# Kernel optimization log

Hardware: AMD Instinct MI355X
Metric: run time of the kernel (lower is better)

The kernel has to match this reference:

```python
import jax, jax.numpy as jnp
import numpy as np

T, D, R = 8192, 2048, 2048

def setup_inputs() -> dict:
    key = jax.random.key(0)
    ks = jax.random.split(key, 5)
    x = jax.random.normal(ks[0], (T, D), jnp.float32)
    h0 = jnp.zeros((R,), jnp.float32)  # initialize_carry()
    W_a = jax.random.normal(ks[1], (D, R), jnp.float32) / np.float32(np.sqrt(D))
    W_b = jax.random.normal(ks[2], (D, R), jnp.float32) / np.float32(np.sqrt(D))
    W_out = jax.random.normal(ks[3], (R, D), jnp.float32) / np.float32(np.sqrt(R))
    W_skip = jax.random.normal(ks[4], (D, D), jnp.float32) / np.float32(np.sqrt(D))
    return {"x": x, "h0": h0, "W_a": W_a, "W_b": W_b, "W_out": W_out, "W_skip": W_skip}


def _combine(e1, e2):
    # semigroup op for diagonal linear recurrence: h' = a2*h + b2
    a1, b1 = e1
    a2, b2 = e2
    return (a1 * a2, a2 * b1 + b2)


def reference(x, h0, W_a, W_b, W_out, W_skip):
    # forward_map (vmapped over time via broadcasting): x_t -> (a_t, b_t)
    a = jax.nn.sigmoid(x @ W_a)        # [T, R] input-dependent decay
    b = (x @ W_b) * (1.0 - a)          # [T, R] gated input injection
    # fold initial carry in as identity-decay element (1, h0), then scan
    ones_row = jnp.ones((1, R), x.dtype)
    a_all = jnp.concatenate([ones_row, a], axis=0)          # [T+1, R]
    b_all = jnp.concatenate([h0[None, :], b], axis=0)       # [T+1, R]
    _, h_all = jax.lax.associative_scan(_combine, (a_all, b_all), axis=0)
    next_h = h_all[1:]                 # [T, R] recurrent states
    # backward_map (vmapped over time): h_t, x_t -> y_t
    y = jnp.tanh(next_h) @ W_out + x @ W_skip   # [T, D]
    return next_h, y
```

## Files before the change

### kernel.cpp

```cpp
#include <hip/hip_runtime.h>
#include <hip/hip_fp16.h>


#define T_DIM 8192
#define D_DIM 2048
#define R_DIM 2048
#define NCH   128
#define LCH   64

typedef _Float16 f16;
typedef _Float16 f16x2 __attribute__((ext_vector_type(2)));
typedef _Float16 f16x4 __attribute__((ext_vector_type(4)));
typedef _Float16 f16x8 __attribute__((ext_vector_type(8)));
typedef float    f32x4 __attribute__((ext_vector_type(4)));

#define AS1 __attribute__((address_space(1)))
#define AS3 __attribute__((address_space(3)))
#define GLOAD_LDS16(g, l) \
  __builtin_amdgcn_global_load_lds((const AS1 void*)(g), (AS3 void*)(l), 16, 0, 0)

__device__ __forceinline__ int swz(int p) { return p ^ (((p >> 7) & 7) << 4); }


__global__ __launch_bounds__(256) void cvt_f32_f16_kernel(
    const float* __restrict__ in, f16* __restrict__ out, int n4) {
  int i = blockIdx.x * 256 + threadIdx.x;
  if (i >= n4) return;
  float4 v = ((const float4*)in)[i];
  f16x4 o; o.x = (f16)v.x; o.y = (f16)v.y; o.z = (f16)v.z; o.w = (f16)v.w;
  ((f16x4*)out)[i] = o;
}

__global__ __launch_bounds__(256) void transpose_cvt_kernel(
    const float* __restrict__ in, f16* __restrict__ out) {
  __shared__ float tile[32][33];
  int bx = blockIdx.x * 32, by = blockIdx.y * 32;
  int tx = threadIdx.x, ty = threadIdx.y;
  #pragma unroll
  for (int i = 0; i < 32; i += 8)
    tile[ty + i][tx] = in[(size_t)(by + ty + i) * 2048 + bx + tx];
  __syncthreads();
  #pragma unroll
  for (int i = 0; i < 32; i += 8)
    out[(size_t)(bx + ty + i) * 2048 + by + tx] = (f16)tile[tx][ty + i];
}

template <int MODE>
__global__ __launch_bounds__(512, 2) void gemm_kernel(
    const f16* __restrict__ A1, const f16* __restrict__ B1, int NT1,
    const f16* __restrict__ A2, const f16* __restrict__ B2, int NT2,
    const f16* __restrict__ aAux, void* __restrict__ outp) {
  __shared__ __align__(16) char lds[4 * 32768];
  const int tid = threadIdx.x;
  const int l = tid & 63, w = tid >> 6;
  const int wrow = w >> 2, wcol = w & 3;
  const int l15 = l & 15, kq = (l >> 4) * 16;

  const int id = blockIdx.x;
  const int sw = (id & 7) * 32 + (id >> 3);
  const int m0 = (sw >> 3) * 256, n0 = (sw & 7) * 256;
  const int NTtot = NT1 + NT2;

  int gOff[2];
  #pragma unroll
  for (int q = 0; q < 2; q++) {
    int p = (q * 512 + tid) * 16 & 16383;
    int lg = swz(p);
    gOff[q] = (lg >> 6) * 4096 + (lg & 63);
  }
  int oA[8], oB[4];
  #pragma unroll
  for (int m = 0; m < 8; m++)
    oA[m] = swz((wrow * 128 + m * 16 + l15) * 64 + kq);
  #pragma unroll
  for (int n = 0; n < 4; n++)
    oB[n] = swz((wcol * 64 + n * 16 + l15) * 64 + kq);

  f32x4 acc[8][4];
  #pragma unroll
  for (int m = 0; m < 8; m++)
    #pragma unroll
    for (int n = 0; n < 4; n++)
      acc[m][n] = (f32x4){0.f, 0.f, 0.f, 0.f};

  auto stage = [&](int tf) {
    const f16* At; const f16* Bt; int kt;
    if (tf < NT1) { At = A1; Bt = B1; kt = tf; }
    else          { At = A2; Bt = B2; kt = tf - NT1; }
    const char* gA = (const char*)(At + (size_t)m0 * 2048 + kt * 32);
    const char* gB = (const char*)(Bt + (size_t)n0 * 2048 + kt * 32);
    char* ldsA = lds + (tf & 3) * 32768;
    char* ldsB = ldsA + 16384;
    #pragma unroll
    for (int q = 0; q < 2; q++) {
      GLOAD_LDS16(gA + gOff[q], ldsA + (q * 512 + w * 64) * 16);
      GLOAD_LDS16(gB + gOff[q], ldsB + (q * 512 + w * 64) * 16);
    }
  };

  stage(0); stage(1); stage(2);

  for (int t = 0; t < NTtot; ++t) {
    const int rem = NTtot - 1 - t;
    if (rem >= 2)      asm volatile("s_waitcnt vmcnt(8)" ::: "memory");
    else if (rem == 1) asm volatile("s_waitcnt vmcnt(4)" ::: "memory");
    else               asm volatile("s_waitcnt vmcnt(0)" ::: "memory");
    asm volatile("s_barrier" ::: "memory");
    if (t + 3 < NTtot) stage(t + 3);

    const char* bA = lds + (t & 3) * 32768;
    const char* bB = bA + 16384;
    f16x8 af[8], bf[4];
    #pragma unroll
    for (int m = 0; m < 8; m++) af[m] = *(const f16x8*)(bA + oA[m]);
    #pragma unroll
    for (int n = 0; n < 4; n++) bf[n] = *(const f16x8*)(bB + oB[n]);
    __builtin_amdgcn_s_setprio(1);
    #pragma unroll
    for (int m = 0; m < 8; m++)
      #pragma unroll
      for (int n = 0; n < 4; n++)
        acc[m][n] = __builtin_amdgcn_mfma_f32_16x16x32_f16(af[m], bf[n], acc[m][n], 0, 0, 0);
    __builtin_amdgcn_s_setprio(0);
  }

  const int r0 = m0 + wrow * 128 + (l >> 4) * 4;
  const int c0 = n0 + wcol * 64 + l15;
  #pragma unroll
  for (int m = 0; m < 8; m++)
    #pragma unroll
    for (int n = 0; n < 4; n++)
      #pragma unroll
      for (int j = 0; j < 4; j++) {
        size_t idx = (size_t)(r0 + m * 16 + j) * 2048 + (c0 + n * 16);
        float v = acc[m][n][j];
        if (MODE == 0) {
          ((float*)outp)[idx] = v;
        } else if (MODE == 1) {
          ((f16*)outp)[idx] = (f16)(1.0f / (1.0f + __expf(-v)));
        } else {
          ((f16*)outp)[idx] = (f16)(v * (1.0f - (float)aAux[idx]));
        }
      }
}


__global__ __launch_bounds__(256) void scan_pass_a(
    const f16* __restrict__ a, const f16* __restrict__ b,
    float* __restrict__ Ac, float* __restrict__ Bc) {
  int tid = blockIdx.x * 256 + threadIdx.x;
  int c  = tid >> 10;
  int r2 = (tid & 1023) << 1;
  const f16* pa = a + (size_t)c * LCH * R_DIM + r2;
  const f16* pb = b + (size_t)c * LCH * R_DIM + r2;
  float A0 = 1.f, B0 = 0.f, A1 = 1.f, B1 = 0.f;
  #pragma unroll 8
  for (int i = 0; i < LCH; i++) {
    f16x2 av = *(const f16x2*)(pa + (size_t)i * R_DIM);
    f16x2 bv = *(const f16x2*)(pb + (size_t)i * R_DIM);
    float a0 = (float)av.x, a1 = (float)av.y;
    B0 = fmaf(a0, B0, (float)bv.x); A0 *= a0;
    B1 = fmaf(a1, B1, (float)bv.y); A1 *= a1;
  }
  size_t o = (size_t)c * R_DIM + r2;
  *(float2*)&Ac[o] = make_float2(A0, A1);
  *(float2*)&Bc[o] = make_float2(B0, B1);
}

__global__ __launch_bounds__(256) void scan_carry(
    const float* __restrict__ Ac, const float* __restrict__ Bc,
    const float* __restrict__ h0, float* __restrict__ carry) {
  int r = blockIdx.x * 256 + threadIdx.x;
  float h = h0[r];
  #pragma unroll 8
  for (int c = 0; c < NCH; c++) {
    size_t o = (size_t)c * R_DIM + r;
    carry[o] = h;
    h = fmaf(Ac[o], h, Bc[o]);
  }
}

__global__ __launch_bounds__(256) void scan_pass_c(
    const f16* __restrict__ a, const f16* __restrict__ b,
    const float* __restrict__ carry,
    float* __restrict__ hout, f16* __restrict__ th) {
  int tid = blockIdx.x * 256 + threadIdx.x;
  int c  = tid >> 10;
  int r2 = (tid & 1023) << 1;
  size_t base = (size_t)c * LCH * R_DIM + r2;
  const f16* pa = a + base;
  const f16* pb = b + base;
  float2 hv = *(const float2*)&carry[(size_t)c * R_DIM + r2];
  float hA = hv.x, hB = hv.y;
  #pragma unroll 4
  for (int i = 0; i < LCH; i++) {
    f16x2 av = *(const f16x2*)(pa + (size_t)i * R_DIM);
    f16x2 bv = *(const f16x2*)(pb + (size_t)i * R_DIM);
    hA = fmaf((float)av.x, hA, (float)bv.x);
    hB = fmaf((float)av.y, hB, (float)bv.y);
    size_t o = base + (size_t)i * R_DIM;
    *(float2*)&hout[o] = make_float2(hA, hB);
    f16x2 tv; tv.x = (f16)tanhf(hA); tv.y = (f16)tanhf(hB);
    *(f16x2*)(th + o) = tv;
  }
}


extern "C" void kernel_launch(void* const* d_in, const int* in_sizes, int n_in,
                              void* d_out, int out_size, void* d_ws, size_t ws_size,
                              hipStream_t stream) {
  const float* x      = (const float*)d_in[0];
  const float* h0     = (const float*)d_in[1];
  const float* W_a    = (const float*)d_in[2];
  const float* W_b    = (const float*)d_in[3];
  const float* W_out  = (const float*)d_in[4];
  const float* W_skip = (const float*)d_in[5];
  float* out_h = (float*)d_out;
  float* out_y = out_h + (size_t)T_DIM * R_DIM;

  char* ws = (char*)d_ws;
  size_t off = 0;
  auto alloc = [&](size_t bytes) -> void* {
    void* p = ws + off;
    off += (bytes + 255) & ~(size_t)255;
    return p;
  };
  f16*  x16   = (f16*)alloc((size_t)T_DIM * D_DIM * 2);
  f16*  WaT   = (f16*)alloc((size_t)D_DIM * R_DIM * 2);
  f16*  WbT   = (f16*)alloc((size_t)D_DIM * R_DIM * 2);
  f16*  WoutT = (f16*)alloc((size_t)R_DIM * D_DIM * 2);
  f16*  WskT  = (f16*)alloc((size_t)D_DIM * D_DIM * 2);
  f16*  a16   = (f16*)alloc((size_t)T_DIM * R_DIM * 2);
  f16*  b16   = (f16*)alloc((size_t)T_DIM * R_DIM * 2);
  f16*  th16  = (f16*)alloc((size_t)T_DIM * R_DIM * 2);
  float* Ac   = (float*)alloc((size_t)NCH * R_DIM * 4);
  float* Bc   = (float*)alloc((size_t)NCH * R_DIM * 4);
  float* carry= (float*)alloc((size_t)NCH * R_DIM * 4);

  {
    int n4 = T_DIM * D_DIM / 4;
    cvt_f32_f16_kernel<<<(n4 + 255) / 256, 256, 0, stream>>>(x, x16, n4);
  }
  dim3 tg(64, 64), tb(32, 8);
  transpose_cvt_kernel<<<tg, tb, 0, stream>>>(W_a,    WaT);
  transpose_cvt_kernel<<<tg, tb, 0, stream>>>(W_b,    WbT);
  transpose_cvt_kernel<<<tg, tb, 0, stream>>>(W_out,  WoutT);
  transpose_cvt_kernel<<<tg, tb, 0, stream>>>(W_skip, WskT);

  const int NT = D_DIM / 32;
  gemm_kernel<1><<<256, 512, 0, stream>>>(x16, WaT, NT, nullptr, nullptr, 0, nullptr, a16);
  gemm_kernel<2><<<256, 512, 0, stream>>>(x16, WbT, NT, nullptr, nullptr, 0, a16,    b16);

  scan_pass_a<<<NCH * (R_DIM / 2) / 256, 256, 0, stream>>>(a16, b16, Ac, Bc);
  scan_carry <<<R_DIM / 256, 256, 0, stream>>>(Ac, Bc, h0, carry);
  scan_pass_c<<<NCH * (R_DIM / 2) / 256, 256, 0, stream>>>(a16, b16, carry, out_h, th16);

  gemm_kernel<0><<<256, 512, 0, stream>>>(th16, WoutT, NT, x16, WskT, NT, nullptr, out_y);
}
```

Baseline: 563.1 us.

## Retile GEMM to 32x32 MFMA with 256x128 tiles and move gating into scan

The GEMM now uses 256x128 block tiles with 32x32x16 MFMAs, triple-buffered LDS and an occupancy target of four blocks. Its epilogue stores raw pre-activations in f16, so the sigmoid and gating are recomputed inside both scan passes and the GEMM no longer rereads the gate tensor. The four weight transposes are merged into one launch, and tanh/sigmoid use fast rcp/exp forms. This cuts launch count and epilogue traffic in exchange for smaller tiles, recomputed transcendentals in the scans, and a possible loss of precision from storing pre-activations in f16.

```diff
diff --git a/kernel.cpp b/kernel.cpp
--- a/kernel.cpp
+++ b/kernel.cpp
@@ -12,7 +12,7 @@
 typedef _Float16 f16x2 __attribute__((ext_vector_type(2)));
 typedef _Float16 f16x4 __attribute__((ext_vector_type(4)));
 typedef _Float16 f16x8 __attribute__((ext_vector_type(8)));
-typedef float    f32x4 __attribute__((ext_vector_type(4)));
+typedef float    f32x16 __attribute__((ext_vector_type(16)));
 
 #define AS1 __attribute__((address_space(1)))
 #define AS3 __attribute__((address_space(3)))
@@ -20,6 +20,13 @@
   __builtin_amdgcn_global_load_lds((const AS1 void*)(g), (AS3 void*)(l), 16, 0, 0)
 
 __device__ __forceinline__ int swz(int p) { return p ^ (((p >> 7) & 7) << 4); }
+
+__device__ __forceinline__ float sigmoid_f(float z) {
+  return __builtin_amdgcn_rcpf(1.0f + __expf(-z));
+}
+__device__ __forceinline__ float tanh_f(float x) {
+  return 1.0f - 2.0f * __builtin_amdgcn_rcpf(1.0f + __expf(2.0f * x));
+}
 
 
 __global__ __launch_bounds__(256) void cvt_f32_f16_kernel(
@@ -32,7 +39,16 @@
 }
 
 __global__ __launch_bounds__(256) void transpose_cvt_kernel(
-    const float* __restrict__ in, f16* __restrict__ out) {
+    const float* __restrict__ s0, f16* __restrict__ d0,
+    const float* __restrict__ s1, f16* __restrict__ d1,
+    const float* __restrict__ s2, f16* __restrict__ d2,
+    const float* __restrict__ s3, f16* __restrict__ d3) {
+  const float* in; f16* out;
+  int z = blockIdx.z;
+  if (z == 0)      { in = s0; out = d0; }
+  else if (z == 1) { in = s1; out = d1; }
+  else if (z == 2) { in = s2; out = d2; }
+  else             { in = s3; out = d3; }
   __shared__ float tile[32][33];
   int bx = blockIdx.x * 32, by = blockIdx.y * 32;
   int tx = threadIdx.x, ty = threadIdx.y;
@@ -46,121 +62,127 @@
 }
 
 template <int MODE>
-__global__ __launch_bounds__(512, 2) void gemm_kernel(
+__global__ __launch_bounds__(512, 4) void gemm_kernel(
     const f16* __restrict__ A1, const f16* __restrict__ B1, int NT1,
     const f16* __restrict__ A2, const f16* __restrict__ B2, int NT2,
-    const f16* __restrict__ aAux, void* __restrict__ outp) {
-  __shared__ __align__(16) char lds[4 * 32768];
+    void* __restrict__ outp) {
+  __shared__ __align__(16) char lds[3 * 24576];
   const int tid = threadIdx.x;
   const int l = tid & 63, w = tid >> 6;
-  const int wrow = w >> 2, wcol = w & 3;
-  const int l15 = l & 15, kq = (l >> 4) * 16;
+  const int wrow = w >> 1, wcol = w & 1;
+  const int l31 = l & 31, hi = l >> 5;
 
   const int id = blockIdx.x;
-  const int sw = (id & 7) * 32 + (id >> 3);
-  const int m0 = (sw >> 3) * 256, n0 = (sw & 7) * 256;
+  const int sw = (id & 7) * 64 + (id >> 3);
+  const int m0 = (sw >> 4) * 256, n0 = (sw & 15) * 128;
   const int NTtot = NT1 + NT2;
 
-  int gOff[2];
-  #pragma unroll
-  for (int q = 0; q < 2; q++) {
-    int p = (q * 512 + tid) * 16 & 16383;
-    int lg = swz(p);
-    gOff[q] = (lg >> 6) * 4096 + (lg & 63);
-  }
-  int oA[8], oB[4];
-  #pragma unroll
-  for (int m = 0; m < 8; m++)
-    oA[m] = swz((wrow * 128 + m * 16 + l15) * 64 + kq);
-  #pragma unroll
-  for (int n = 0; n < 4; n++)
-    oB[n] = swz((wcol * 64 + n * 16 + l15) * 64 + kq);
-
-  f32x4 acc[8][4];
-  #pragma unroll
-  for (int m = 0; m < 8; m++)
-    #pragma unroll
-    for (int n = 0; n < 4; n++)
-      acc[m][n] = (f32x4){0.f, 0.f, 0.f, 0.f};
-
-  auto stage = [&](int tf) {
+  int gA0, gA1, gB0;
+  {
+    int p0 = tid * 16;
+    int p1 = (512 + tid) * 16;
+    int pb = tid * 16;
+    int lg;
+    lg = swz(p0); gA0 = (lg >> 6) * 4096 + (lg & 63);
+    lg = swz(p1); gA1 = (lg >> 6) * 4096 + (lg & 63);
+    lg = swz(pb); gB0 = (lg >> 6) * 4096 + (lg & 63);
+  }
+  int oA[2][2], oB[2][2];
+  #pragma unroll
+  for (int m = 0; m < 2; m++)
+    #pragma unroll
+    for (int kk = 0; kk < 2; kk++)
+      oA[m][kk] = swz((wrow * 64 + m * 32 + l31) * 64 + kk * 32 + hi * 16);
+  #pragma unroll
+  for (int n = 0; n < 2; n++)
+    #pragma unroll
+    for (int kk = 0; kk < 2; kk++)
+      oB[n][kk] = swz((wcol * 64 + n * 32 + l31) * 64 + kk * 32 + hi * 16);
+
+  f32x16 acc[2][2];
+  #pragma unroll
+  for (int m = 0; m < 2; m++)
+    #pragma unroll
+    for (int n = 0; n < 2; n++)
+      #pragma unroll
+      for (int r = 0; r < 16; r++)
+        acc[m][n][r] = 0.f;
+
+  auto stage = [&](int tf, int slot) {
     const f16* At; const f16* Bt; int kt;
     if (tf < NT1) { At = A1; Bt = B1; kt = tf; }
     else          { At = A2; Bt = B2; kt = tf - NT1; }
-    const char* gA = (const char*)(At + (size_t)m0 * 2048 + kt * 32);
-    const char* gB = (const char*)(Bt + (size_t)n0 * 2048 + kt * 32);
-    char* ldsA = lds + (tf & 3) * 32768;
-    char* ldsB = ldsA + 16384;
-    #pragma unroll
-    for (int q = 0; q < 2; q++) {
-      GLOAD_LDS16(gA + gOff[q], ldsA + (q * 512 + w * 64) * 16);
-      GLOAD_LDS16(gB + gOff[q], ldsB + (q * 512 + w * 64) * 16);
-    }
+    const char* gA = (const char*)At + (size_t)m0 * 4096 + kt * 64;
+    const char* gB = (const char*)Bt + (size_t)n0 * 4096 + kt * 64;
+    char* dA = lds + slot * 24576;
+    char* dB = dA + 16384;
+    GLOAD_LDS16(gA + gA0, dA + (w * 64) * 16);
+    GLOAD_LDS16(gA + gA1, dA + (512 + w * 64) * 16);
+    GLOAD_LDS16(gB + gB0, dB + (w * 64) * 16);
   };
 
-  stage(0); stage(1); stage(2);
-
+  stage(0, 0); stage(1, 1);
+  int cs = 0;
   for (int t = 0; t < NTtot; ++t) {
-    const int rem = NTtot - 1 - t;
-    if (rem >= 2)      asm volatile("s_waitcnt vmcnt(8)" ::: "memory");
-    else if (rem == 1) asm volatile("s_waitcnt vmcnt(4)" ::: "memory");
+    if (t < NTtot - 1) asm volatile("s_waitcnt vmcnt(3)" ::: "memory");
     else               asm volatile("s_waitcnt vmcnt(0)" ::: "memory");
     asm volatile("s_barrier" ::: "memory");
-    if (t + 3 < NTtot) stage(t + 3);
-
-    const char* bA = lds + (t & 3) * 32768;
+    if (t + 2 < NTtot) {
+      int ss = cs + 2; if (ss >= 3) ss -= 3;
+      stage(t + 2, ss);
+    }
+    const char* bA = lds + cs * 24576;
     const char* bB = bA + 16384;
-    f16x8 af[8], bf[4];
-    #pragma unroll
-    for (int m = 0; m < 8; m++) af[m] = *(const f16x8*)(bA + oA[m]);
-    #pragma unroll
-    for (int n = 0; n < 4; n++) bf[n] = *(const f16x8*)(bB + oB[n]);
     __builtin_amdgcn_s_setprio(1);
     #pragma unroll
-    for (int m = 0; m < 8; m++)
+    for (int kk = 0; kk < 2; kk++) {
+      f16x8 a0 = *(const f16x8*)(bA + oA[0][kk]);
+      f16x8 a1 = *(const f16x8*)(bA + oA[1][kk]);
+      f16x8 b0 = *(const f16x8*)(bB + oB[0][kk]);
+      f16x8 b1 = *(const f16x8*)(bB + oB[1][kk]);
+      acc[0][0] = __builtin_amdgcn_mfma_f32_32x32x16_f16(a0, b0, acc[0][0], 0, 0, 0);
+      acc[0][1] = __builtin_amdgcn_mfma_f32_32x32x16_f16(a0, b1, acc[0][1], 0, 0, 0);
+      acc[1][0] = __builtin_amdgcn_mfma_f32_32x32x16_f16(a1, b0, acc[1][0], 0, 0, 0);
+      acc[1][1] = __builtin_amdgcn_mfma_f32_32x32x16_f16(a1, b1, acc[1][1], 0, 0, 0);
+    }
+    __builtin_amdgcn_s_setprio(0);
+    cs = (cs == 2) ? 0 : cs + 1;
+  }
+
+  const int r0 = m0 + wrow * 64 + 4 * hi;
+  const int c0 = n0 + wcol * 64 + l31;
+  #pragma unroll
+  for (int m = 0; m < 2; m++)
+    #pragma unroll
+    for (int n = 0; n < 2; n++)
       #pragma unroll
-      for (int n = 0; n < 4; n++)
-        acc[m][n] = __builtin_amdgcn_mfma_f32_16x16x32_f16(af[m], bf[n], acc[m][n], 0, 0, 0);
-    __builtin_amdgcn_s_setprio(0);
-  }
-
-  const int r0 = m0 + wrow * 128 + (l >> 4) * 4;
-  const int c0 = n0 + wcol * 64 + l15;
-  #pragma unroll
-  for (int m = 0; m < 8; m++)
-    #pragma unroll
-    for (int n = 0; n < 4; n++)
-      #pragma unroll
-      for (int j = 0; j < 4; j++) {
-        size_t idx = (size_t)(r0 + m * 16 + j) * 2048 + (c0 + n * 16);
-        float v = acc[m][n][j];
-        if (MODE == 0) {
-          ((float*)outp)[idx] = v;
-        } else if (MODE == 1) {
-          ((f16*)outp)[idx] = (f16)(1.0f / (1.0f + __expf(-v)));
-        } else {
-          ((f16*)outp)[idx] = (f16)(v * (1.0f - (float)aAux[idx]));
-        }
+      for (int r = 0; r < 16; r++) {
+        int row = r0 + m * 32 + (r & 3) + 8 * (r >> 2);
+        size_t idx = (size_t)row * 2048 + (c0 + n * 32);
+        float v = acc[m][n][r];
+        if (MODE == 0) ((float*)outp)[idx] = v;
+        else           ((f16*)outp)[idx]   = (f16)v;
       }
 }
 
 
 __global__ __launch_bounds__(256) void scan_pass_a(
-    const f16* __restrict__ a, const f16* __restrict__ b,
+    const f16* __restrict__ za, const f16* __restrict__ zb,
     float* __restrict__ Ac, float* __restrict__ Bc) {
   int tid = blockIdx.x * 256 + threadIdx.x;
   int c  = tid >> 10;
   int r2 = (tid & 1023) << 1;
-  const f16* pa = a + (size_t)c * LCH * R_DIM + r2;
-  const f16* pb = b + (size_t)c * LCH * R_DIM + r2;
+  const f16* pa = za + (size_t)c * LCH * R_DIM + r2;
+  const f16* pb = zb + (size_t)c * LCH * R_DIM + r2;
   float A0 = 1.f, B0 = 0.f, A1 = 1.f, B1 = 0.f;
   #pragma unroll 8
   for (int i = 0; i < LCH; i++) {
     f16x2 av = *(const f16x2*)(pa + (size_t)i * R_DIM);
     f16x2 bv = *(const f16x2*)(pb + (size_t)i * R_DIM);
-    float a0 = (float)av.x, a1 = (float)av.y;
-    B0 = fmaf(a0, B0, (float)bv.x); A0 *= a0;
-    B1 = fmaf(a1, B1, (float)bv.y); A1 *= a1;
+    float a0 = sigmoid_f((float)av.x), a1 = sigmoid_f((float)av.y);
+    float b0 = (float)bv.x * (1.0f - a0), b1 = (float)bv.y * (1.0f - a1);
+    B0 = fmaf(a0, B0, b0); A0 *= a0;
+    B1 = fmaf(a1, B1, b1); A1 *= a1;
   }
   size_t o = (size_t)c * R_DIM + r2;
   *(float2*)&Ac[o] = make_float2(A0, A1);
@@ -181,26 +203,27 @@
 }
 
 __global__ __launch_bounds__(256) void scan_pass_c(
-    const f16* __restrict__ a, const f16* __restrict__ b,
+    const f16* __restrict__ za, const f16* __restrict__ zb,
     const float* __restrict__ carry,
     float* __restrict__ hout, f16* __restrict__ th) {
   int tid = blockIdx.x * 256 + threadIdx.x;
   int c  = tid >> 10;
   int r2 = (tid & 1023) << 1;
   size_t base = (size_t)c * LCH * R_DIM + r2;
-  const f16* pa = a + base;
-  const f16* pb = b + base;
+  const f16* pa = za + base;
+  const f16* pb = zb + base;
   float2 hv = *(const float2*)&carry[(size_t)c * R_DIM + r2];
   float hA = hv.x, hB = hv.y;
   #pragma unroll 4
   for (int i = 0; i < LCH; i++) {
     f16x2 av = *(const f16x2*)(pa + (size_t)i * R_DIM);
     f16x2 bv = *(const f16x2*)(pb + (size_t)i * R_DIM);
-    hA = fmaf((float)av.x, hA, (float)bv.x);
-    hB = fmaf((float)av.y, hB, (float)bv.y);
+    float a0 = sigmoid_f((float)av.x), a1 = sigmoid_f((float)av.y);
+    hA = fmaf(a0, hA, (float)bv.x * (1.0f - a0));
+    hB = fmaf(a1, hB, (float)bv.y * (1.0f - a1));
     size_t o = base + (size_t)i * R_DIM;
     *(float2*)&hout[o] = make_float2(hA, hB);
-    f16x2 tv; tv.x = (f16)tanhf(hA); tv.y = (f16)tanhf(hB);
+    f16x2 tv; tv.x = (f16)tanh_f(hA); tv.y = (f16)tanh_f(hB);
     *(f16x2*)(th + o) = tv;
   }
 }
@@ -230,8 +253,8 @@
   f16*  WbT   = (f16*)alloc((size_t)D_DIM * R_DIM * 2);
   f16*  WoutT = (f16*)alloc((size_t)R_DIM * D_DIM * 2);
   f16*  WskT  = (f16*)alloc((size_t)D_DIM * D_DIM * 2);
-  f16*  a16   = (f16*)alloc((size_t)T_DIM * R_DIM * 2);
-  f16*  b16   = (f16*)alloc((size_t)T_DIM * R_DIM * 2);
+  f16*  za16  = (f16*)alloc((size_t)T_DIM * R_DIM * 2);
+  f16*  zb16  = (f16*)alloc((size_t)T_DIM * R_DIM * 2);
   f16*  th16  = (f16*)alloc((size_t)T_DIM * R_DIM * 2);
   float* Ac   = (float*)alloc((size_t)NCH * R_DIM * 4);
   float* Bc   = (float*)alloc((size_t)NCH * R_DIM * 4);
@@ -241,19 +264,19 @@
     int n4 = T_DIM * D_DIM / 4;
     cvt_f32_f16_kernel<<<(n4 + 255) / 256, 256, 0, stream>>>(x, x16, n4);
   }
-  dim3 tg(64, 64), tb(32, 8);
-  transpose_cvt_kernel<<<tg, tb, 0, stream>>>(W_a,    WaT);
-  transpose_cvt_kernel<<<tg, tb, 0, stream>>>(W_b,    WbT);
-  transpose_cvt_kernel<<<tg, tb, 0, stream>>>(W_out,  WoutT);
-  transpose_cvt_kernel<<<tg, tb, 0, stream>>>(W_skip, WskT);
+  {
+    dim3 tg(64, 64, 4), tb(32, 8);
+    transpose_cvt_kernel<<<tg, tb, 0, stream>>>(W_a, WaT, W_b, WbT,
+                                                W_out, WoutT, W_skip, WskT);
+  }
 
   const int NT = D_DIM / 32;
-  gemm_kernel<1><<<256, 512, 0, stream>>>(x16, WaT, NT, nullptr, nullptr, 0, nullptr, a16);
-  gemm_kernel<2><<<256, 512, 0, stream>>>(x16, WbT, NT, nullptr, nullptr, 0, a16,    b16);
-
-  scan_pass_a<<<NCH * (R_DIM / 2) / 256, 256, 0, stream>>>(a16, b16, Ac, Bc);
+  gemm_kernel<1><<<512, 512, 0, stream>>>(x16, WaT, NT, nullptr, nullptr, 0, za16);
+  gemm_kernel<1><<<512, 512, 0, stream>>>(x16, WbT, NT, nullptr, nullptr, 0, zb16);
+
+  scan_pass_a<<<NCH * (R_DIM / 2) / 256, 256, 0, stream>>>(za16, zb16, Ac, Bc);
   scan_carry <<<R_DIM / 256, 256, 0, stream>>>(Ac, Bc, h0, carry);
-  scan_pass_c<<<NCH * (R_DIM / 2) / 256, 256, 0, stream>>>(a16, b16, carry, out_h, th16);
-
-  gemm_kernel<0><<<256, 512, 0, stream>>>(th16, WoutT, NT, x16, WskT, NT, nullptr, out_y);
-}
+  scan_pass_c<<<NCH * (R_DIM / 2) / 256, 256, 0, stream>>>(za16, zb16, carry, out_h, th16);
+
+  gemm_kernel<0><<<512, 512, 0, stream>>>(th16, WoutT, NT, x16, WskT, NT, out_y);
+}
```

Result: slower. 636.5 us (+13.0%).
